# Optimization experiments

Hardware: AMD Instinct MI355X
Metric: run time of the kernel (lower is better)

## Reference

```python
import jax, jax.numpy as jnp
import numpy as np

P = 30           # max_pad_size
S = 224          # image_size
CROP = S - 2 * P # 164
B = 16
T = 16


def _interp1d(out_pos, in_size, out_size, base):
    """PyTorch bilinear (align_corners=False) 1D source indices/weights.
    out_pos: float32 positions local to the region; out_size: traced int scalar;
    in_size: static python int; base: static offset into a concatenated source.
    Returns (i0, i1, w) with i0,i1 in [base, base+in_size).
    """
    scale = jnp.float32(in_size) / out_size.astype(jnp.float32)
    f = jnp.maximum((out_pos + 0.5) * scale - 0.5, 0.0)
    i0 = jnp.floor(f).astype(jnp.int32)
    w = f - i0.astype(jnp.float32)
    i1 = jnp.minimum(i0 + 1, in_size - 1)
    return i0 + base, i1 + base, w


def _make_prompt(pu, pd, pl, pr, off_r, off_d):
    # pu [3,2P,S], pd [3,P,S], pl [3,CROP,2P], pr [3,CROP,P]
    off_l = 2 * P - off_r
    off_u = 2 * P - off_d

    # ---- horizontal: build middle rows [3, CROP, S] = [pad_left | zeros | pad_right]
    j = jnp.arange(S, dtype=jnp.int32)
    jf = j.astype(jnp.float32)
    src_h = jnp.concatenate([pl, pr], axis=-1)  # [3, CROP, 3P]
    i0l, i1l, wl = _interp1d(jf, 2 * P, off_l, 0)
    i0r, i1r, wr = _interp1d(jf - (S - off_r).astype(jnp.float32), P, off_r, 2 * P)
    mL = j < off_l
    mR = j >= S - off_r
    idx0 = jnp.where(mL, i0l, i0r)
    idx1 = jnp.where(mL, i1l, i1r)
    w = jnp.where(mL, wl, wr)
    mid = src_h[:, :, idx0] * (1.0 - w) + src_h[:, :, idx1] * w
    mid = jnp.where((mL | mR)[None, None, :], mid, 0.0)  # [3, CROP, S]

    # ---- vertical: [pad_up ; mid ; pad_down] -> [3, S, S]
    cat_v = jnp.concatenate([pu, pd, mid], axis=1)  # [3, 3P+CROP, S]
    i = jnp.arange(S, dtype=jnp.int32)
    if_ = i.astype(jnp.float32)
    i0u, i1u, wu = _interp1d(if_, 2 * P, off_u, 0)
    i0d, i1d, wd = _interp1d(if_ - (S - off_d).astype(jnp.float32), P, off_d, 2 * P)
    mid_idx = i - off_u + 3 * P  # middle rows copied verbatim (weight 0)
    mU = i < off_u
    mD = i >= S - off_d
    r0 = jnp.where(mU, i0u, jnp.where(mD, i0d, mid_idx))
    r1 = jnp.where(mU, i1u, jnp.where(mD, i1d, mid_idx))
    wv = jnp.where(mU, wu, jnp.where(mD, wd, 0.0))
    return cat_v[:, r0, :] * (1.0 - wv)[None, :, None] + cat_v[:, r1, :] * wv[None, :, None]


def setup_inputs() -> dict:
    key = jax.random.key(0)
    ks = jax.random.split(key, 8)
    x = jax.random.normal(ks[0], (B, 3, T, S, S), dtype=jnp.float32)
    pad_up = jax.random.normal(ks[1], (3, 3, 2 * P, S), dtype=jnp.float32)
    pad_down = jax.random.normal(ks[2], (3, 3, P, S), dtype=jnp.float32)
    pad_left = jax.random.normal(ks[3], (3, 3, CROP, 2 * P), dtype=jnp.float32)
    pad_right = jax.random.normal(ks[4], (3, 3, CROP, P), dtype=jnp.float32)
    cam_views = jax.random.randint(ks[5], (B,), 0, 3, dtype=jnp.int32)
    offsets_right = jax.random.randint(ks[6], (B,), 1, P + 1, dtype=jnp.int32)
    offsets_down = jax.random.randint(ks[7], (B,), 1, P + 1, dtype=jnp.int32)
    return {"x": x, "pad_up": pad_up, "pad_down": pad_down, "pad_left": pad_left,
            "pad_right": pad_right, "cam_views": cam_views,
            "offsets_right": offsets_right, "offsets_down": offsets_down}


def reference(x, pad_up, pad_down, pad_left, pad_right, cam_views, offsets_right, offsets_down):
    def per_sample(cam, orr, od):
        return _make_prompt(pad_up[cam], pad_down[cam], pad_left[cam], pad_right[cam], orr, od)

    prompt = jax.vmap(per_sample)(cam_views, offsets_right, offsets_down)  # [B,3,S,S]
    return x + prompt[:, :, None, :, :]  # broadcast over T frames
```

## Files before the change

### kernel.cpp

```cpp
#include <hip/hip_runtime.h>


#define PP 30
#define SS 224
#define CROPC 164
#define BB 16
#define TT 16

__device__ __forceinline__ void interp1d(float pos, float in_size, int in_size_i,
                                         int out_size, int& i0, int& i1, float& w) {
    float scale = in_size / (float)out_size;
    float f = fmaxf((pos + 0.5f) * scale - 0.5f, 0.0f);
    i0 = (int)floorf(f);
    w = f - (float)i0;
    i1 = min(i0 + 1, in_size_i - 1);
}

__global__ void __launch_bounds__(256)
prompt_add_kernel(const float* __restrict__ x,
                  const float* __restrict__ pu,
                  const float* __restrict__ pd,
                  const float* __restrict__ pl,
                  const float* __restrict__ pr,
                  const int* __restrict__ cam_views,
                  const int* __restrict__ offs_r,
                  const int* __restrict__ offs_d,
                  float* __restrict__ out) {
    const int J4 = SS / 4;
    int idx = blockIdx.x * blockDim.x + threadIdx.x;
    const int total = BB * 3 * SS * J4;
    if (idx >= total) return;

    int j4 = idx % J4;
    int tmp = idx / J4;
    int i = tmp % SS;
    tmp /= SS;
    int c = tmp % 3;
    int b = tmp / 3;

    const int cam = cam_views[b];
    const int off_r = offs_r[b];
    const int off_d = offs_d[b];
    const int off_l = 2 * PP - off_r;
    const int off_u = 2 * PP - off_d;

    const float* puc = pu + (size_t)(cam * 3 + c) * (2 * PP) * SS;
    const float* pdc = pd + (size_t)(cam * 3 + c) * PP * SS;
    const float* plc = pl + (size_t)(cam * 3 + c) * CROPC * (2 * PP);
    const float* prc = pr + (size_t)(cam * 3 + c) * CROPC * PP;

    const int j0 = j4 * 4;
    float pv[4];

    if (i < off_u) {
        int r0, r1; float w;
        interp1d((float)i, (float)(2 * PP), 2 * PP, off_u, r0, r1, w);
        const float* a = puc + (size_t)r0 * SS + j0;
        const float* bp = puc + (size_t)r1 * SS + j0;
        #pragma unroll
        for (int k = 0; k < 4; k++)
            pv[k] = a[k] * (1.0f - w) + bp[k] * w;
    } else if (i >= SS - off_d) {
        int r0, r1; float w;
        interp1d((float)(i - (SS - off_d)), (float)PP, PP, off_d, r0, r1, w);
        const float* a = pdc + (size_t)r0 * SS + j0;
        const float* bp = pdc + (size_t)r1 * SS + j0;
        #pragma unroll
        for (int k = 0; k < 4; k++)
            pv[k] = a[k] * (1.0f - w) + bp[k] * w;
    } else {
        const int r = i - off_u;
        const float* plr = plc + (size_t)r * (2 * PP);
        const float* prr = prc + (size_t)r * PP;
        #pragma unroll
        for (int k = 0; k < 4; k++) {
            int j = j0 + k;
            float v = 0.0f;
            if (j < off_l) {
                int c0, c1; float w;
                interp1d((float)j, (float)(2 * PP), 2 * PP, off_l, c0, c1, w);
                v = plr[c0] * (1.0f - w) + plr[c1] * w;
            } else if (j >= SS - off_r) {
                int c0, c1; float w;
                interp1d((float)(j - (SS - off_r)), (float)PP, PP, off_r, c0, c1, w);
                v = prr[c0] * (1.0f - w) + prr[c1] * w;
            }
            pv[k] = v;
        }
    }

    size_t base = ((size_t)(b * 3 + c) * TT) * (SS * SS) + (size_t)i * SS + j0;
    #pragma unroll
    for (int t = 0; t < TT; t++) {
        size_t off = base + (size_t)t * (SS * SS);
        float4 xv = *reinterpret_cast<const float4*>(x + off);
        float4 ov;
        ov.x = xv.x + pv[0];
        ov.y = xv.y + pv[1];
        ov.z = xv.z + pv[2];
        ov.w = xv.w + pv[3];
        *reinterpret_cast<float4*>(out + off) = ov;
    }
}

extern "C" void kernel_launch(void* const* d_in, const int* in_sizes, int n_in,
                              void* d_out, int out_size, void* d_ws, size_t ws_size,
                              hipStream_t stream) {
    const float* x  = (const float*)d_in[0];
    const float* pu = (const float*)d_in[1];
    const float* pd = (const float*)d_in[2];
    const float* pl = (const float*)d_in[3];
    const float* pr = (const float*)d_in[4];
    const int* cam  = (const int*)d_in[5];
    const int* orr  = (const int*)d_in[6];
    const int* od   = (const int*)d_in[7];
    float* out = (float*)d_out;

    const int total = BB * 3 * SS * (SS / 4);
    const int threads = 256;
    const int blocks = (total + threads - 1) / threads;
    prompt_add_kernel<<<blocks, threads, 0, stream>>>(x, pu, pd, pl, pr, cam, orr, od, out);
}
```

Before: 280.2 us.

## Split into prompt-build and flat streaming add kernels using workspace

Precomputes the per-sample prompt image into the workspace with a small kernel, then runs a flat, fully parallel streaming kernel that adds it to every frame of x. The goal is to replace the per-thread 16-frame strided loop with many independent coalesced float4 accesses, for better memory-level parallelism. It costs an extra launch and a round trip of the prompt through memory, and keeps the fused kernel as a fallback when the workspace is too small.

```diff
diff --git a/kernel.cpp b/kernel.cpp
--- a/kernel.cpp
+++ b/kernel.cpp
@@ -17,15 +17,14 @@
 }
 
 __global__ void __launch_bounds__(256)
-prompt_add_kernel(const float* __restrict__ x,
-                  const float* __restrict__ pu,
-                  const float* __restrict__ pd,
-                  const float* __restrict__ pl,
-                  const float* __restrict__ pr,
-                  const int* __restrict__ cam_views,
-                  const int* __restrict__ offs_r,
-                  const int* __restrict__ offs_d,
-                  float* __restrict__ out) {
+prompt_build_kernel(const float* __restrict__ pu,
+                    const float* __restrict__ pd,
+                    const float* __restrict__ pl,
+                    const float* __restrict__ pr,
+                    const int* __restrict__ cam_views,
+                    const int* __restrict__ offs_r,
+                    const int* __restrict__ offs_d,
+                    float* __restrict__ prompt) {
     const int J4 = SS / 4;
     int idx = blockIdx.x * blockDim.x + threadIdx.x;
     const int total = BB * 3 * SS * J4;
@@ -89,16 +88,100 @@
         }
     }
 
+    float4 o; o.x = pv[0]; o.y = pv[1]; o.z = pv[2]; o.w = pv[3];
+    *reinterpret_cast<float4*>(prompt + (size_t)idx * 4) = o;
+}
+
+__global__ void __launch_bounds__(256)
+stream_add_kernel(const float* __restrict__ x,
+                  const float* __restrict__ prompt,
+                  float* __restrict__ out) {
+    const int P4 = SS * SS / 4;
+    int idx = blockIdx.x * blockDim.x + threadIdx.x;
+    int p4 = idx % P4;
+    int frame = idx / P4;
+    int bc = frame / TT;
+
+    const float4 xv = *reinterpret_cast<const float4*>(x + (size_t)idx * 4);
+    const float4 pv = *reinterpret_cast<const float4*>(prompt + ((size_t)bc * P4 + p4) * 4);
+    float4 ov;
+    ov.x = xv.x + pv.x;
+    ov.y = xv.y + pv.y;
+    ov.z = xv.z + pv.z;
+    ov.w = xv.w + pv.w;
+    *reinterpret_cast<float4*>(out + (size_t)idx * 4) = ov;
+}
+
+__global__ void __launch_bounds__(256)
+fused_kernel(const float* __restrict__ x,
+             const float* __restrict__ pu, const float* __restrict__ pd,
+             const float* __restrict__ pl, const float* __restrict__ pr,
+             const int* __restrict__ cam_views,
+             const int* __restrict__ offs_r, const int* __restrict__ offs_d,
+             float* __restrict__ out) {
+    const int J4 = SS / 4;
+    int idx = blockIdx.x * blockDim.x + threadIdx.x;
+    const int total = BB * 3 * SS * J4;
+    if (idx >= total) return;
+    int j4 = idx % J4;
+    int tmp = idx / J4;
+    int i = tmp % SS;
+    tmp /= SS;
+    int c = tmp % 3;
+    int b = tmp / 3;
+    const int cam = cam_views[b];
+    const int off_r = offs_r[b];
+    const int off_d = offs_d[b];
+    const int off_l = 2 * PP - off_r;
+    const int off_u = 2 * PP - off_d;
+    const float* puc = pu + (size_t)(cam * 3 + c) * (2 * PP) * SS;
+    const float* pdc = pd + (size_t)(cam * 3 + c) * PP * SS;
+    const float* plc = pl + (size_t)(cam * 3 + c) * CROPC * (2 * PP);
+    const float* prc = pr + (size_t)(cam * 3 + c) * CROPC * PP;
+    const int j0 = j4 * 4;
+    float pv[4];
+    if (i < off_u) {
+        int r0, r1; float w;
+        interp1d((float)i, (float)(2 * PP), 2 * PP, off_u, r0, r1, w);
+        const float* a = puc + (size_t)r0 * SS + j0;
+        const float* bp = puc + (size_t)r1 * SS + j0;
+        #pragma unroll
+        for (int k = 0; k < 4; k++) pv[k] = a[k] * (1.0f - w) + bp[k] * w;
+    } else if (i >= SS - off_d) {
+        int r0, r1; float w;
+        interp1d((float)(i - (SS - off_d)), (float)PP, PP, off_d, r0, r1, w);
+        const float* a = pdc + (size_t)r0 * SS + j0;
+        const float* bp = pdc + (size_t)r1 * SS + j0;
+        #pragma unroll
+        for (int k = 0; k < 4; k++) pv[k] = a[k] * (1.0f - w) + bp[k] * w;
+    } else {
+        const int r = i - off_u;
+        const float* plr = plc + (size_t)r * (2 * PP);
+        const float* prr = prc + (size_t)r * PP;
+        #pragma unroll
+        for (int k = 0; k < 4; k++) {
+            int j = j0 + k;
+            float v = 0.0f;
+            if (j < off_l) {
+                int c0, c1; float w;
+                interp1d((float)j, (float)(2 * PP), 2 * PP, off_l, c0, c1, w);
+                v = plr[c0] * (1.0f - w) + plr[c1] * w;
+            } else if (j >= SS - off_r) {
+                int c0, c1; float w;
+                interp1d((float)(j - (SS - off_r)), (float)PP, PP, off_r, c0, c1, w);
+                v = prr[c0] * (1.0f - w) + prr[c1] * w;
+            }
+            pv[k] = v;
+        }
+    }
     size_t base = ((size_t)(b * 3 + c) * TT) * (SS * SS) + (size_t)i * SS + j0;
     #pragma unroll
     for (int t = 0; t < TT; t++) {
         size_t off = base + (size_t)t * (SS * SS);
         float4 xv = *reinterpret_cast<const float4*>(x + off);
         float4 ov;
-        ov.x = xv.x + pv[0];
-        ov.y = xv.y + pv[1];
-        ov.z = xv.z + pv[2];
-        ov.w = xv.w + pv[3];
+        ov.x = xv.x + pv[0]; ov.y = xv.y + pv[1];
+        ov.z = xv.z + pv[2]; ov.w = xv.w + pv[3];
         *reinterpret_cast<float4*>(out + off) = ov;
     }
 }
@@ -116,8 +199,18 @@
     const int* od   = (const int*)d_in[7];
     float* out = (float*)d_out;
 
-    const int total = BB * 3 * SS * (SS / 4);
-    const int threads = 256;
-    const int blocks = (total + threads - 1) / threads;
-    prompt_add_kernel<<<blocks, threads, 0, stream>>>(x, pu, pd, pl, pr, cam, orr, od, out);
-}
+    const size_t prompt_bytes = (size_t)BB * 3 * SS * SS * sizeof(float);
+
+    if (ws_size >= prompt_bytes) {
+        float* prompt = (float*)d_ws;
+        const int total_p = BB * 3 * SS * (SS / 4);
+        prompt_build_kernel<<<(total_p + 255) / 256, 256, 0, stream>>>(
+            pu, pd, pl, pr, cam, orr, od, prompt);
+        const int total_s = BB * 3 * TT * SS * (SS / 4);
+        stream_add_kernel<<<(total_s + 255) / 256, 256, 0, stream>>>(x, prompt, out);
+    } else {
+        const int total = BB * 3 * SS * (SS / 4);
+        fused_kernel<<<(total + 255) / 256, 256, 0, stream>>>(
+            x, pu, pd, pl, pr, cam, orr, od, out);
+    }
+}
```

Measured after the change: 273.3 us. 2.5% less time.
